# Performance work log

Measured on AMD Instinct MI355X. Metric: run time of the kernel, lower is better.

Reference implementation:

```python
import jax, jax.numpy as jnp
import numpy as np

WS = 7          # window size (7x7)
N = WS * WS     # tokens per window = 49
C = 192         # channels
H = 6           # heads
NW = 64         # windows per image (for mask)
B_ = 8192       # num_windows * batch


def _rel_index():
    coords = np.stack(np.meshgrid(np.arange(WS), np.arange(WS), indexing='ij'))  # [2,7,7]
    cf = coords.reshape(2, -1)                       # [2,49]
    rc = (cf[:, :, None] - cf[:, None, :]).transpose(1, 2, 0).astype(np.int64)  # [49,49,2]
    rc[..., 0] += WS - 1
    rc[..., 1] += WS - 1
    rc[..., 0] *= 2 * WS - 1
    return jnp.asarray(rc.sum(-1), dtype=jnp.int32)  # [49,49], values in [0, 169)


def setup_inputs() -> dict:
    key = jax.random.key(0)
    ks = jax.random.split(key, 10)
    std = 0.02
    return {
        'xq': jax.random.normal(ks[0], (B_, N, C), dtype=jnp.float32),
        'mask': jax.random.normal(ks[1], (NW, N, N), dtype=jnp.float32),
        'Wq': jax.random.normal(ks[2], (C, C), dtype=jnp.float32) * std,
        'bq': jnp.zeros((C,), dtype=jnp.float32),
        'Wkv': jax.random.normal(ks[3], (C, 2 * C), dtype=jnp.float32) * std,
        'bkv': jnp.zeros((2 * C,), dtype=jnp.float32),
        'Wproj': jax.random.normal(ks[4], (C, C), dtype=jnp.float32) * std,
        'bproj': jnp.zeros((C,), dtype=jnp.float32),
        'bias_table': jax.random.normal(ks[5], ((2 * WS - 1) * (2 * WS - 1), H), dtype=jnp.float32) * std,
        'rel_index': _rel_index(),
    }


def reference(xq, mask, Wq, bq, Wkv, bkv, Wproj, bproj, bias_table, rel_index):
    b_, n, c = xq.shape
    h = H
    dh = c // h
    scale = dh ** (-0.5)
    # projections (xkv = xq since xkv is None in the original call)
    q = (xq @ Wq + bq).reshape(b_, n, h, dh).transpose(0, 2, 1, 3) * scale      # [b_,h,n,dh]
    kv = (xq @ Wkv + bkv).reshape(b_, n, 2, h, dh).transpose(2, 0, 3, 1, 4)     # [2,b_,h,n,dh]
    k, v = kv[0], kv[1]
    attn = jnp.einsum('bhqd,bhkd->bhqk', q, k)                                   # [b_,h,n,n]
    # gathered relative-position bias: [n,n,h] -> [h,n,n]
    bias = bias_table[rel_index.reshape(-1)].reshape(n, n, h).transpose(2, 0, 1)
    attn = attn + bias[None]
    # mask add: [b_//nw, nw, h, n, n] + [1, nw, 1, n, n]
    nw = mask.shape[0]
    attn = attn.reshape(b_ // nw, nw, h, n, n) + mask[None, :, None]
    attn = jax.nn.softmax(attn.reshape(b_, h, n, n), axis=-1)
    x = jnp.einsum('bhqk,bhkd->bhqd', attn, v).transpose(0, 2, 1, 3).reshape(b_, n, c)
    return x @ Wproj + bproj
```

## Files before the change

kernel.cpp:

```cpp
#include <hip/hip_runtime.h>


#define NTOK 49
#define CCH 192

typedef __bf16 bf16_t;
typedef bf16_t bf16x8 __attribute__((ext_vector_type(8)));
typedef bf16_t bf16x4 __attribute__((ext_vector_type(4)));
typedef float f32x4 __attribute__((ext_vector_type(4)));

#define WS_WQT   0
#define WS_WKVT  73728
#define WS_WPT   221184
#define WS_BQS   294912
#define WS_TBL   295680

#define SWZ(row, off) ((off) ^ (((row) & 7) << 4))

__global__ void prep_kernel(const float* __restrict__ Wq, const float* __restrict__ bq,
                            const float* __restrict__ Wkv, const float* __restrict__ Wproj,
                            const float* __restrict__ btab, const int* __restrict__ rel,
                            const float* __restrict__ mask,
                            bf16_t* __restrict__ wqt, bf16_t* __restrict__ wkvt,
                            bf16_t* __restrict__ wpt, float* __restrict__ bqs,
                            float* __restrict__ tbl, int mode) {
    const float SC = 0.17677669529663687f;
    long i = (long)blockIdx.x * 256 + threadIdx.x;
    if (i < 36864) { int n = i / 192, k = i % 192; wqt[i] = (bf16_t)(Wq[k * 192 + n] * SC); return; }
    i -= 36864;
    if (i < 73728) { int n = i / 192, k = i % 192; wkvt[i] = (bf16_t)Wkv[k * 384 + n]; return; }
    i -= 73728;
    if (i < 36864) { int n = i / 192, k = i % 192; wpt[i] = (bf16_t)Wproj[k * 192 + n]; return; }
    i -= 36864;
    if (i < 192) { bqs[i] = bq[i] * SC; return; }
    i -= 192;
    if (mode == 0) {
        if (i < 979072) {
            int c = i % 52; long r = i / 52; int q = r % 49; r /= 49; int h = r % 6; int w = r / 6;
            tbl[i] = (c < 49) ? (btab[rel[q * 49 + c] * 6 + h] + mask[(size_t)w * 2401 + q * 49 + c]) : 0.f;
        }
    } else if (mode == 1) {
        if (i < 15288) { int c = i % 52; int r = i / 52; int q = r % 49; int h = r / 49;
            tbl[i] = (c < 49) ? btab[rel[q * 49 + c] * 6 + h] : 0.f; return; }
        i -= 15288;
        if (i < 163072) { int c = i % 52; long r = i / 52; int q = r % 49; int w = r / 49;
            tbl[15288 + i] = (c < 49) ? mask[(size_t)w * 2401 + q * 49 + c] : 0.f; }
    } else {
        if (i < 14406) { int h = i / 2401, rc = i % 2401; tbl[i] = btab[rel[rc] * 6 + h]; }
    }
}

__global__ __launch_bounds__(1024, 4) void wattn_kernel(
    const float* __restrict__ xq, const float* __restrict__ mask,
    const float* __restrict__ bkv, const float* __restrict__ bproj,
    const bf16_t* __restrict__ wqt, const bf16_t* __restrict__ wkvt, const bf16_t* __restrict__ wpt,
    const float* __restrict__ bqs, const float* __restrict__ tbl,
    float* __restrict__ out, int mode)
{
    __shared__ __align__(16) unsigned char smem[131072];
    unsigned char* XsO = smem;
    unsigned char* Qs  = smem + 24576;
    unsigned char* Ks  = smem + 49152;
    unsigned char* Vt  = smem + 73728;
    unsigned char* Ps  = smem + 98304;

    const int tid = threadIdx.x;
    const int wid = tid >> 6;
    const int lane = tid & 63;
    const int l15 = lane & 15;
    const int lg = lane >> 4;
    const int b = blockIdx.x;
    const float* xp = xq + (size_t)b * (NTOK * CCH);

    for (int idx = tid; idx < 2352; idx += 1024) {
        int row = idx / 48;
        int c4 = idx % 48;
        float4 v = *(const float4*)(xp + row * 192 + c4 * 4);
        bf16x4 pk = { (bf16_t)v.x, (bf16_t)v.y, (bf16_t)v.z, (bf16_t)v.w };
        *(bf16x4*)(XsO + row * 384 + SWZ(row, c4 * 8)) = pk;
    }
    if (tid < 720) *(unsigned long long*)(XsO + 49 * 384 + tid * 8) = 0ULL;
    __syncthreads();

    {
        bf16x8 bfr[6];
        float4 bias4;
        float bv = 0.f;
        int prev_ut = -1;
        for (int u = 9 * wid; u < 9 * wid + 9; ++u) {
            int ut = u >> 2, mt = u & 3;
            bool isV = (ut >= 24);
            if (ut != prev_ut) {
                prev_ut = ut;
                const bf16_t* wrow;
                if (ut < 12)      wrow = wqt  + (size_t)(ut * 16 + l15) * 192;
                else if (ut < 24) wrow = wkvt + (size_t)((ut - 12) * 16 + l15) * 192;
                else              wrow = wkvt + (size_t)(192 + (ut - 24) * 16 + l15) * 192;
#pragma unroll
                for (int ks = 0; ks < 6; ks++) bfr[ks] = *(const bf16x8*)(wrow + ks * 32 + lg * 8);
                if (!isV) {
                    const float* bp = (ut < 12) ? (bqs + ut * 16) : (bkv + (ut - 12) * 16);
                    bias4 = *(const float4*)(bp + lg * 4);
                } else {
                    bv = bkv[192 + (ut - 24) * 16 + l15];
                }
            }
            int xrow = mt * 16 + l15;
            bf16x8 xf[6];
#pragma unroll
            for (int ks = 0; ks < 6; ks++)
                xf[ks] = *(const bf16x8*)(XsO + xrow * 384 + SWZ(xrow, ks * 64 + lg * 16));
            if (!isV) {
                f32x4 acc = { bias4.x, bias4.y, bias4.z, bias4.w };
#pragma unroll
                for (int ks = 0; ks < 6; ks++)
                    acc = __builtin_amdgcn_mfma_f32_16x16x32_bf16(bfr[ks], xf[ks], acc, 0, 0, 0);
                int ncol = (ut < 12 ? ut : ut - 12) * 16;
                unsigned char* dst = (ut < 12) ? Qs : Ks;
                bf16x4 pk = { (bf16_t)acc[0], (bf16_t)acc[1], (bf16_t)acc[2], (bf16_t)acc[3] };
                int trow = mt * 16 + l15;
                *(bf16x4*)(dst + trow * 384 + SWZ(trow, ncol * 2 + lg * 8)) = pk;
            } else {
                f32x4 acc = { bv, bv, bv, bv };
#pragma unroll
                for (int ks = 0; ks < 6; ks++)
                    acc = __builtin_amdgcn_mfma_f32_16x16x32_bf16(xf[ks], bfr[ks], acc, 0, 0, 0);
                int crow = (ut - 24) * 16 + l15;
                bf16x4 pk = { (bf16_t)acc[0], (bf16_t)acc[1], (bf16_t)acc[2], (bf16_t)acc[3] };
                *(bf16x4*)(Vt + crow * 128 + SWZ(crow, mt * 32 + lg * 8)) = pk;
            }
        }
    }
    __syncthreads();

    const int widx = b & 63;
    unsigned char* Pw = Ps + wid * 2048;
    for (int u = wid; u < 24; u += 16) {
        int h = u >> 2, qt = u & 3;
        int cb = h * 64 + lg * 16;
        int qrow = qt * 16 + l15;
        bf16x8 qfr = *(const bf16x8*)(Qs + qrow * 384 + SWZ(qrow, cb));
        f32x4 s[4];
#pragma unroll
        for (int f = 0; f < 4; f++) {
            int kr = f * 16 + l15;
            bf16x8 kfr = *(const bf16x8*)(Ks + kr * 384 + SWZ(kr, cb));
            f32x4 z = { 0.f, 0.f, 0.f, 0.f };
            s[f] = __builtin_amdgcn_mfma_f32_16x16x32_bf16(kfr, qfr, z, 0, 0, 0);
        }
        int q = qt * 16 + l15;
        bool qok = (q < 49);
#pragma unroll
        for (int f = 0; f < 4; f++) {
            int kb = f * 16 + lg * 4;
            float4 a = { 0.f, 0.f, 0.f, 0.f };
            if (qok && kb < 49) {
                if (mode == 0) {
                    a = *(const float4*)(tbl + (((size_t)(widx * 6 + h) * 49 + q) * 52 + kb));
                } else if (mode == 1) {
                    float4 b1 = *(const float4*)(tbl + ((size_t)(h * 49 + q) * 52 + kb));
                    float4 m1 = *(const float4*)(tbl + 15288 + (((size_t)widx * 49 + q) * 52 + kb));
                    a.x = b1.x + m1.x; a.y = b1.y + m1.y; a.z = b1.z + m1.z; a.w = b1.w + m1.w;
                }
            }
#pragma unroll
            for (int j = 0; j < 4; j++) {
                int k = kb + j;
                float av = (j == 0) ? a.x : (j == 1) ? a.y : (j == 2) ? a.z : a.w;
                if (mode == 2) {
                    av = 0.f;
                    if (qok && k < 49)
                        av = tbl[h * 2401 + q * 49 + k] + mask[(size_t)widx * 2401 + q * 49 + k];
                }
                if (k >= 49) s[f][j] = -1e30f;
                else if (qok) s[f][j] += av;
            }
        }
        float m = -1e30f;
#pragma unroll
        for (int f = 0; f < 4; f++)
#pragma unroll
            for (int j = 0; j < 4; j++) m = fmaxf(m, s[f][j]);
        m = fmaxf(m, __shfl_xor(m, 16));
        m = fmaxf(m, __shfl_xor(m, 32));
        float t = 0.f;
#pragma unroll
        for (int f = 0; f < 4; f++)
#pragma unroll
            for (int j = 0; j < 4; j++) { s[f][j] = __expf(s[f][j] - m); t += s[f][j]; }
        t += __shfl_xor(t, 16);
        t += __shfl_xor(t, 32);
        float inv = 1.0f / t;
#pragma unroll
        for (int f = 0; f < 4; f++) {
            bf16x4 pk = { (bf16_t)(s[f][0] * inv), (bf16_t)(s[f][1] * inv),
                          (bf16_t)(s[f][2] * inv), (bf16_t)(s[f][3] * inv) };
            *(bf16x4*)(Pw + l15 * 128 + SWZ(l15, f * 32 + lg * 8)) = pk;
        }
        __threadfence_block();
        bf16x8 pa[2];
#pragma unroll
        for (int ks = 0; ks < 2; ks++)
            pa[ks] = *(const bf16x8*)(Pw + l15 * 128 + SWZ(l15, ks * 64 + lg * 16));
#pragma unroll
        for (int dt = 0; dt < 2; dt++) {
            f32x4 acc = { 0.f, 0.f, 0.f, 0.f };
#pragma unroll
            for (int ks = 0; ks < 2; ks++) {
                int vr = h * 32 + dt * 16 + l15;
                bf16x8 vfr = *(const bf16x8*)(Vt + vr * 128 + SWZ(vr, ks * 64 + lg * 16));
                acc = __builtin_amdgcn_mfma_f32_16x16x32_bf16(vfr, pa[ks], acc, 0, 0, 0);
            }
            int orow = qt * 16 + l15;
            bf16x4 pk = { (bf16_t)acc[0], (bf16_t)acc[1], (bf16_t)acc[2], (bf16_t)acc[3] };
            *(bf16x4*)(XsO + orow * 384 + SWZ(orow, h * 64 + dt * 32 + lg * 8)) = pk;
        }
    }
    __syncthreads();

    {
        float* op = out + (size_t)b * (NTOK * CCH);
        bf16x8 bfr[6];
        float4 bias4 = { 0.f, 0.f, 0.f, 0.f };
        int prev_nt = -1;
        for (int u = 3 * wid; u < 3 * wid + 3; ++u) {
            int nt = u >> 2, mt = u & 3;
            if (nt != prev_nt) {
                prev_nt = nt;
                const bf16_t* wrow = wpt + (size_t)(nt * 16 + l15) * 192;
#pragma unroll
                for (int ks = 0; ks < 6; ks++) bfr[ks] = *(const bf16x8*)(wrow + ks * 32 + lg * 8);
                bias4 = *(const float4*)(bproj + nt * 16 + lg * 4);
            }
            int orow = mt * 16 + l15;
            f32x4 acc = { bias4.x, bias4.y, bias4.z, bias4.w };
#pragma unroll
            for (int ks = 0; ks < 6; ks++) {
                bf16x8 of = *(const bf16x8*)(XsO + orow * 384 + SWZ(orow, ks * 64 + lg * 16));
                acc = __builtin_amdgcn_mfma_f32_16x16x32_bf16(bfr[ks], of, acc, 0, 0, 0);
            }
            if (orow < 49) {
                float4 st = { acc[0], acc[1], acc[2], acc[3] };
                *(float4*)(op + orow * 192 + nt * 16 + lg * 4) = st;
            }
        }
    }
}

extern "C" void kernel_launch(void* const* d_in, const int* in_sizes, int n_in,
                              void* d_out, int out_size, void* d_ws, size_t ws_size,
                              hipStream_t stream) {
    const float* xq    = (const float*)d_in[0];
    const float* mask  = (const float*)d_in[1];
    const float* Wq    = (const float*)d_in[2];
    const float* bq    = (const float*)d_in[3];
    const float* Wkv   = (const float*)d_in[4];
    const float* bkv   = (const float*)d_in[5];
    const float* Wproj = (const float*)d_in[6];
    const float* bproj = (const float*)d_in[7];
    const float* btab  = (const float*)d_in[8];
    const int*   rel   = (const int*)d_in[9];
    float* out = (float*)d_out;

    char* ws = (char*)d_ws;
    bf16_t* wqt  = (bf16_t*)(ws + WS_WQT);
    bf16_t* wkvt = (bf16_t*)(ws + WS_WKVT);
    bf16_t* wpt  = (bf16_t*)(ws + WS_WPT);
    float*  bqs  = (float*)(ws + WS_BQS);
    float*  tbl  = (float*)(ws + WS_TBL);

    size_t need0 = (size_t)WS_TBL + 979072u * 4u;
    size_t need1 = (size_t)WS_TBL + 178360u * 4u;
    int mode = (ws_size >= need0) ? 0 : (ws_size >= need1 ? 1 : 2);

    long prep_elems = 147648L + (mode == 0 ? 979072L : (mode == 1 ? 178360L : 14406L));
    int prep_blocks = (int)((prep_elems + 255) / 256);
    prep_kernel<<<prep_blocks, 256, 0, stream>>>(Wq, bq, Wkv, Wproj, btab, rel, mask,
                                                 wqt, wkvt, wpt, bqs, tbl, mode);
    wattn_kernel<<<8192, 1024, 0, stream>>>(xq, mask, bkv, bproj, wqt, wkvt, wpt,
                                            bqs, tbl, out, mode);
}
```

Measured before the change: 642.4 us.

## Keep Q and P in registers via shuffles, shrink LDS, use exp2 softmax

Each wave now computes Q for its own query tile and keeps it in registers, moving it into MFMA operand layout with lane shuffles instead of staging through shared memory. The softmax probabilities are shuffled into operand form the same way, so the P buffer disappears. Shared memory drops from 128KB to 72KB and the launch-bounds occupancy hint is raised, which should let more blocks share a CU. The prep kernel folds log2(e) into the Q scale and the bias/mask table, pads the table rows to 64 with a -inf pad so the padding mask is precomputed, and the kernel uses exp2, rcp and deferred normalization after PV. The costs are extra shuffle traffic and register pressure, and weight fragments are reloaded per tile rather than reused.

```diff
diff --git a/kernel.cpp b/kernel.cpp
--- a/kernel.cpp
+++ b/kernel.cpp
@@ -7,6 +7,7 @@
 typedef __bf16 bf16_t;
 typedef bf16_t bf16x8 __attribute__((ext_vector_type(8)));
 typedef bf16_t bf16x4 __attribute__((ext_vector_type(4)));
+typedef bf16_t bf16x2 __attribute__((ext_vector_type(2)));
 typedef float f32x4 __attribute__((ext_vector_type(4)));
 
 #define WS_WQT   0
@@ -16,6 +17,11 @@
 #define WS_TBL   295680
 
 #define SWZ(row, off) ((off) ^ (((row) & 7) << 4))
+
+__device__ __forceinline__ unsigned pk2(float a, float b) {
+    bf16x2 w = { (bf16_t)a, (bf16_t)b };
+    return __builtin_bit_cast(unsigned, w);
+}
 
 __global__ void prep_kernel(const float* __restrict__ Wq, const float* __restrict__ bq,
                             const float* __restrict__ Wkv, const float* __restrict__ Wproj,
@@ -24,7 +30,8 @@
                             bf16_t* __restrict__ wqt, bf16_t* __restrict__ wkvt,
                             bf16_t* __restrict__ wpt, float* __restrict__ bqs,
                             float* __restrict__ tbl, int mode) {
-    const float SC = 0.17677669529663687f;
+    const float SC  = 0.2550718212080052f;
+    const float L2E = 1.4426950408889634f;
     long i = (long)blockIdx.x * 256 + threadIdx.x;
     if (i < 36864) { int n = i / 192, k = i % 192; wqt[i] = (bf16_t)(Wq[k * 192 + n] * SC); return; }
     i -= 36864;
@@ -35,34 +42,33 @@
     if (i < 192) { bqs[i] = bq[i] * SC; return; }
     i -= 192;
     if (mode == 0) {
-        if (i < 979072) {
-            int c = i % 52; long r = i / 52; int q = r % 49; r /= 49; int h = r % 6; int w = r / 6;
-            tbl[i] = (c < 49) ? (btab[rel[q * 49 + c] * 6 + h] + mask[(size_t)w * 2401 + q * 49 + c]) : 0.f;
+        if (i < 1204224) {
+            int c = i & 63; long r = i >> 6; int q = r % 49; r /= 49; int h = r % 6; int w = r / 6;
+            tbl[i] = (c < 49) ? (btab[rel[q * 49 + c] * 6 + h] + mask[(size_t)w * 2401 + q * 49 + c]) * L2E
+                              : -1e30f;
         }
     } else if (mode == 1) {
-        if (i < 15288) { int c = i % 52; int r = i / 52; int q = r % 49; int h = r / 49;
-            tbl[i] = (c < 49) ? btab[rel[q * 49 + c] * 6 + h] : 0.f; return; }
-        i -= 15288;
-        if (i < 163072) { int c = i % 52; long r = i / 52; int q = r % 49; int w = r / 49;
-            tbl[15288 + i] = (c < 49) ? mask[(size_t)w * 2401 + q * 49 + c] : 0.f; }
+        if (i < 18816) { int c = i & 63; int r = i >> 6; int q = r % 49; int h = r / 49;
+            tbl[i] = (c < 49) ? btab[rel[q * 49 + c] * 6 + h] * L2E : 0.f; return; }
+        i -= 18816;
+        if (i < 200704) { int c = i & 63; long r = i >> 6; int q = r % 49; int w = r / 49;
+            tbl[18816 + i] = (c < 49) ? mask[(size_t)w * 2401 + q * 49 + c] * L2E : -1e30f; }
     } else {
         if (i < 14406) { int h = i / 2401, rc = i % 2401; tbl[i] = btab[rel[rc] * 6 + h]; }
     }
 }
 
-__global__ __launch_bounds__(1024, 4) void wattn_kernel(
+__global__ __launch_bounds__(1024, 8) void wattn_kernel(
     const float* __restrict__ xq, const float* __restrict__ mask,
     const float* __restrict__ bkv, const float* __restrict__ bproj,
     const bf16_t* __restrict__ wqt, const bf16_t* __restrict__ wkvt, const bf16_t* __restrict__ wpt,
     const float* __restrict__ bqs, const float* __restrict__ tbl,
     float* __restrict__ out, int mode)
 {
-    __shared__ __align__(16) unsigned char smem[131072];
+    __shared__ __align__(16) unsigned char smem[73728];
     unsigned char* XsO = smem;
-    unsigned char* Qs  = smem + 24576;
-    unsigned char* Ks  = smem + 49152;
-    unsigned char* Vt  = smem + 73728;
-    unsigned char* Ps  = smem + 98304;
+    unsigned char* Ks  = smem + 24576;
+    unsigned char* Vt  = smem + 49152;
 
     const int tid = threadIdx.x;
     const int wid = tid >> 6;
@@ -71,6 +77,7 @@
     const int lg = lane >> 4;
     const int b = blockIdx.x;
     const float* xp = xq + (size_t)b * (NTOK * CCH);
+    const float LOG2E = 1.4426950408889634f;
 
     for (int idx = tid; idx < 2352; idx += 1024) {
         int row = idx / 48;
@@ -82,101 +89,118 @@
     if (tid < 720) *(unsigned long long*)(XsO + 49 * 384 + tid * 8) = 0ULL;
     __syncthreads();
 
+    const int qt = wid & 3;
+    unsigned qw0[4], qw1[4];
     {
-        bf16x8 bfr[6];
-        float4 bias4;
-        float bv = 0.f;
-        int prev_ut = -1;
-        for (int u = 9 * wid; u < 9 * wid + 9; ++u) {
-            int ut = u >> 2, mt = u & 3;
-            bool isV = (ut >= 24);
-            if (ut != prev_ut) {
-                prev_ut = ut;
-                const bf16_t* wrow;
-                if (ut < 12)      wrow = wqt  + (size_t)(ut * 16 + l15) * 192;
-                else if (ut < 24) wrow = wkvt + (size_t)((ut - 12) * 16 + l15) * 192;
-                else              wrow = wkvt + (size_t)(192 + (ut - 24) * 16 + l15) * 192;
-#pragma unroll
-                for (int ks = 0; ks < 6; ks++) bfr[ks] = *(const bf16x8*)(wrow + ks * 32 + lg * 8);
-                if (!isV) {
-                    const float* bp = (ut < 12) ? (bqs + ut * 16) : (bkv + (ut - 12) * 16);
-                    bias4 = *(const float4*)(bp + lg * 4);
-                } else {
-                    bv = bkv[192 + (ut - 24) * 16 + l15];
+        int xrow = qt * 16 + l15;
+        bf16x8 xf[6];
+#pragma unroll
+        for (int ks = 0; ks < 6; ks++)
+            xf[ks] = *(const bf16x8*)(XsO + xrow * 384 + SWZ(xrow, ks * 64 + lg * 16));
+
+        auto qproj = [&](int h, unsigned* qwv) {
+#pragma unroll
+            for (int dlt = 0; dlt < 2; dlt++) {
+                int ut = 2 * h + dlt;
+                float4 b4 = *(const float4*)(bqs + ut * 16 + lg * 4);
+                f32x4 acc = { b4.x, b4.y, b4.z, b4.w };
+                const bf16_t* wr = wqt + (size_t)(ut * 16 + l15) * 192 + lg * 8;
+#pragma unroll
+                for (int ks = 0; ks < 6; ks++) {
+                    bf16x8 bfr = *(const bf16x8*)(wr + ks * 32);
+                    acc = __builtin_amdgcn_mfma_f32_16x16x32_bf16(bfr, xf[ks], acc, 0, 0, 0);
                 }
-            }
-            int xrow = mt * 16 + l15;
-            bf16x8 xf[6];
-#pragma unroll
-            for (int ks = 0; ks < 6; ks++)
-                xf[ks] = *(const bf16x8*)(XsO + xrow * 384 + SWZ(xrow, ks * 64 + lg * 16));
-            if (!isV) {
-                f32x4 acc = { bias4.x, bias4.y, bias4.z, bias4.w };
-#pragma unroll
-                for (int ks = 0; ks < 6; ks++)
-                    acc = __builtin_amdgcn_mfma_f32_16x16x32_bf16(bfr[ks], xf[ks], acc, 0, 0, 0);
-                int ncol = (ut < 12 ? ut : ut - 12) * 16;
-                unsigned char* dst = (ut < 12) ? Qs : Ks;
-                bf16x4 pk = { (bf16_t)acc[0], (bf16_t)acc[1], (bf16_t)acc[2], (bf16_t)acc[3] };
-                int trow = mt * 16 + l15;
-                *(bf16x4*)(dst + trow * 384 + SWZ(trow, ncol * 2 + lg * 8)) = pk;
-            } else {
-                f32x4 acc = { bv, bv, bv, bv };
-#pragma unroll
-                for (int ks = 0; ks < 6; ks++)
-                    acc = __builtin_amdgcn_mfma_f32_16x16x32_bf16(xf[ks], bfr[ks], acc, 0, 0, 0);
-                int crow = (ut - 24) * 16 + l15;
-                bf16x4 pk = { (bf16_t)acc[0], (bf16_t)acc[1], (bf16_t)acc[2], (bf16_t)acc[3] };
-                *(bf16x4*)(Vt + crow * 128 + SWZ(crow, mt * 32 + lg * 8)) = pk;
-            }
-        }
+                qwv[dlt * 2 + 0] = pk2(acc[0], acc[1]);
+                qwv[dlt * 2 + 1] = pk2(acc[2], acc[3]);
+            }
+        };
+        qproj(wid >> 2, qw0);
+        if (wid < 8) qproj(4 + (wid >> 2), qw1);
+    }
+    for (int i = 0; i < 3; i++) {
+        int u = 3 * wid + i;
+        int nt = u >> 2, mt = u & 3;
+        int xr = mt * 16 + l15;
+        bf16x8 xfk[6];
+#pragma unroll
+        for (int ks = 0; ks < 6; ks++)
+            xfk[ks] = *(const bf16x8*)(XsO + xr * 384 + SWZ(xr, ks * 64 + lg * 16));
+        float4 kb4 = *(const float4*)(bkv + nt * 16 + lg * 4);
+        f32x4 ka = { kb4.x, kb4.y, kb4.z, kb4.w };
+        const bf16_t* wrk = wkvt + (size_t)(nt * 16 + l15) * 192 + lg * 8;
+#pragma unroll
+        for (int ks = 0; ks < 6; ks++) {
+            bf16x8 bfr = *(const bf16x8*)(wrk + ks * 32);
+            ka = __builtin_amdgcn_mfma_f32_16x16x32_bf16(bfr, xfk[ks], ka, 0, 0, 0);
+        }
+        bf16x4 kp = { (bf16_t)ka[0], (bf16_t)ka[1], (bf16_t)ka[2], (bf16_t)ka[3] };
+        *(bf16x4*)(Ks + xr * 384 + SWZ(xr, nt * 32 + lg * 8)) = kp;
+        float bv = bkv[192 + nt * 16 + l15];
+        f32x4 va = { bv, bv, bv, bv };
+        const bf16_t* wrv = wkvt + (size_t)(192 + nt * 16 + l15) * 192 + lg * 8;
+#pragma unroll
+        for (int ks = 0; ks < 6; ks++) {
+            bf16x8 bfr = *(const bf16x8*)(wrv + ks * 32);
+            va = __builtin_amdgcn_mfma_f32_16x16x32_bf16(xfk[ks], bfr, va, 0, 0, 0);
+        }
+        int vr = nt * 16 + l15;
+        bf16x4 vp = { (bf16_t)va[0], (bf16_t)va[1], (bf16_t)va[2], (bf16_t)va[3] };
+        *(bf16x4*)(Vt + vr * 128 + SWZ(vr, mt * 32 + lg * 8)) = vp;
     }
     __syncthreads();
 
     const int widx = b & 63;
-    unsigned char* Pw = Ps + wid * 2048;
-    for (int u = wid; u < 24; u += 16) {
-        int h = u >> 2, qt = u & 3;
-        int cb = h * 64 + lg * 16;
-        int qrow = qt * 16 + l15;
-        bf16x8 qfr = *(const bf16x8*)(Qs + qrow * 384 + SWZ(qrow, cb));
+    auto attn_unit = [&](int h, const unsigned* qwv) {
+        unsigned qword[4];
+#pragma unroll
+        for (int i = 0; i < 4; i++) {
+            int src = l15 + 16 * (((lg & 1) << 1) | (i >> 1));
+            unsigned v0 = (unsigned)__shfl((int)qwv[(i & 1)], src, 64);
+            unsigned v1 = (unsigned)__shfl((int)qwv[2 + (i & 1)], src, 64);
+            qword[i] = (lg & 2) ? v1 : v0;
+        }
+        uint4 qq = { qword[0], qword[1], qword[2], qword[3] };
+        bf16x8 qfr = __builtin_bit_cast(bf16x8, qq);
         f32x4 s[4];
 #pragma unroll
         for (int f = 0; f < 4; f++) {
             int kr = f * 16 + l15;
-            bf16x8 kfr = *(const bf16x8*)(Ks + kr * 384 + SWZ(kr, cb));
+            bf16x8 kfr = *(const bf16x8*)(Ks + kr * 384 + SWZ(kr, h * 64 + lg * 16));
             f32x4 z = { 0.f, 0.f, 0.f, 0.f };
             s[f] = __builtin_amdgcn_mfma_f32_16x16x32_bf16(kfr, qfr, z, 0, 0, 0);
         }
         int q = qt * 16 + l15;
         bool qok = (q < 49);
-#pragma unroll
-        for (int f = 0; f < 4; f++) {
-            int kb = f * 16 + lg * 4;
-            float4 a = { 0.f, 0.f, 0.f, 0.f };
-            if (qok && kb < 49) {
-                if (mode == 0) {
-                    a = *(const float4*)(tbl + (((size_t)(widx * 6 + h) * 49 + q) * 52 + kb));
-                } else if (mode == 1) {
-                    float4 b1 = *(const float4*)(tbl + ((size_t)(h * 49 + q) * 52 + kb));
-                    float4 m1 = *(const float4*)(tbl + 15288 + (((size_t)widx * 49 + q) * 52 + kb));
-                    a.x = b1.x + m1.x; a.y = b1.y + m1.y; a.z = b1.z + m1.z; a.w = b1.w + m1.w;
+        if (mode == 0) {
+#pragma unroll
+            for (int f = 0; f < 4; f++) {
+                if (qok) {
+                    float4 bm = *(const float4*)(tbl + (((size_t)(widx * 6 + h) * 49 + q) << 6) + f * 16 + lg * 4);
+                    s[f][0] += bm.x; s[f][1] += bm.y; s[f][2] += bm.z; s[f][3] += bm.w;
                 }
             }
-#pragma unroll
-            for (int j = 0; j < 4; j++) {
-                int k = kb + j;
-                float av = (j == 0) ? a.x : (j == 1) ? a.y : (j == 2) ? a.z : a.w;
-                if (mode == 2) {
-                    av = 0.f;
-                    if (qok && k < 49)
-                        av = tbl[h * 2401 + q * 49 + k] + mask[(size_t)widx * 2401 + q * 49 + k];
+        } else if (mode == 1) {
+#pragma unroll
+            for (int f = 0; f < 4; f++) {
+                if (qok) {
+                    float4 b1 = *(const float4*)(tbl + (((size_t)(h * 49 + q)) << 6) + f * 16 + lg * 4);
+                    float4 m1 = *(const float4*)(tbl + 18816 + (((size_t)(widx * 49 + q)) << 6) + f * 16 + lg * 4);
+                    s[f][0] += b1.x + m1.x; s[f][1] += b1.y + m1.y;
+                    s[f][2] += b1.z + m1.z; s[f][3] += b1.w + m1.w;
                 }
-                if (k >= 49) s[f][j] = -1e30f;
-                else if (qok) s[f][j] += av;
-            }
-        }
-        float m = -1e30f;
+            }
+        } else {
+#pragma unroll
+            for (int f = 0; f < 4; f++)
+#pragma unroll
+                for (int j = 0; j < 4; j++) {
+                    int k = f * 16 + lg * 4 + j;
+                    if (k >= 49) s[f][j] = -1e30f;
+                    else if (qok)
+                        s[f][j] += (tbl[h * 2401 + q * 49 + k] + mask[(size_t)widx * 2401 + q * 49 + k]) * LOG2E;
+                }
+        }
+        float m = s[0][0];
 #pragma unroll
         for (int f = 0; f < 4; f++)
 #pragma unroll
@@ -187,57 +211,63 @@
 #pragma unroll
         for (int f = 0; f < 4; f++)
 #pragma unroll
-            for (int j = 0; j < 4; j++) { s[f][j] = __expf(s[f][j] - m); t += s[f][j]; }
+            for (int j = 0; j < 4; j++) { s[f][j] = __builtin_amdgcn_exp2f(s[f][j] - m); t += s[f][j]; }
         t += __shfl_xor(t, 16);
         t += __shfl_xor(t, 32);
-        float inv = 1.0f / t;
+        float inv = __builtin_amdgcn_rcpf(t);
+        unsigned Wp[8];
 #pragma unroll
         for (int f = 0; f < 4; f++) {
-            bf16x4 pk = { (bf16_t)(s[f][0] * inv), (bf16_t)(s[f][1] * inv),
-                          (bf16_t)(s[f][2] * inv), (bf16_t)(s[f][3] * inv) };
-            *(bf16x4*)(Pw + l15 * 128 + SWZ(l15, f * 32 + lg * 8)) = pk;
-        }
-        __threadfence_block();
+            Wp[f * 2 + 0] = pk2(s[f][0], s[f][1]);
+            Wp[f * 2 + 1] = pk2(s[f][2], s[f][3]);
+        }
         bf16x8 pa[2];
 #pragma unroll
-        for (int ks = 0; ks < 2; ks++)
-            pa[ks] = *(const bf16x8*)(Pw + l15 * 128 + SWZ(l15, ks * 64 + lg * 16));
+        for (int ks2 = 0; ks2 < 2; ks2++) {
+            unsigned pw[4];
+#pragma unroll
+            for (int p = 0; p < 4; p++) {
+                int src = l15 + 16 * (((lg & 1) << 1) | (p >> 1));
+                unsigned v0 = (unsigned)__shfl((int)Wp[(2 * ks2) * 2 + (p & 1)], src, 64);
+                unsigned v1 = (unsigned)__shfl((int)Wp[(2 * ks2 + 1) * 2 + (p & 1)], src, 64);
+                pw[p] = (lg & 2) ? v1 : v0;
+            }
+            uint4 pp = { pw[0], pw[1], pw[2], pw[3] };
+            pa[ks2] = __builtin_bit_cast(bf16x8, pp);
+        }
 #pragma unroll
         for (int dt = 0; dt < 2; dt++) {
             f32x4 acc = { 0.f, 0.f, 0.f, 0.f };
 #pragma unroll
-            for (int ks = 0; ks < 2; ks++) {
+            for (int ks2 = 0; ks2 < 2; ks2++) {
                 int vr = h * 32 + dt * 16 + l15;
-                bf16x8 vfr = *(const bf16x8*)(Vt + vr * 128 + SWZ(vr, ks * 64 + lg * 16));
-                acc = __builtin_amdgcn_mfma_f32_16x16x32_bf16(vfr, pa[ks], acc, 0, 0, 0);
+                bf16x8 vfr = *(const bf16x8*)(Vt + vr * 128 + SWZ(vr, ks2 * 64 + lg * 16));
+                acc = __builtin_amdgcn_mfma_f32_16x16x32_bf16(vfr, pa[ks2], acc, 0, 0, 0);
             }
             int orow = qt * 16 + l15;
-            bf16x4 pk = { (bf16_t)acc[0], (bf16_t)acc[1], (bf16_t)acc[2], (bf16_t)acc[3] };
-            *(bf16x4*)(XsO + orow * 384 + SWZ(orow, h * 64 + dt * 32 + lg * 8)) = pk;
-        }
-    }
+            bf16x4 op4 = { (bf16_t)(acc[0] * inv), (bf16_t)(acc[1] * inv),
+                           (bf16_t)(acc[2] * inv), (bf16_t)(acc[3] * inv) };
+            *(bf16x4*)(XsO + orow * 384 + SWZ(orow, h * 64 + dt * 32 + lg * 8)) = op4;
+        }
+    };
+    attn_unit(wid >> 2, qw0);
+    if (wid < 8) attn_unit(4 + (wid >> 2), qw1);
     __syncthreads();
 
     {
         float* op = out + (size_t)b * (NTOK * CCH);
-        bf16x8 bfr[6];
-        float4 bias4 = { 0.f, 0.f, 0.f, 0.f };
-        int prev_nt = -1;
-        for (int u = 3 * wid; u < 3 * wid + 3; ++u) {
+        for (int i = 0; i < 3; i++) {
+            int u = 3 * wid + i;
             int nt = u >> 2, mt = u & 3;
-            if (nt != prev_nt) {
-                prev_nt = nt;
-                const bf16_t* wrow = wpt + (size_t)(nt * 16 + l15) * 192;
-#pragma unroll
-                for (int ks = 0; ks < 6; ks++) bfr[ks] = *(const bf16x8*)(wrow + ks * 32 + lg * 8);
-                bias4 = *(const float4*)(bproj + nt * 16 + lg * 4);
-            }
+            float4 b4 = *(const float4*)(bproj + nt * 16 + lg * 4);
+            f32x4 acc = { b4.x, b4.y, b4.z, b4.w };
+            const bf16_t* wr = wpt + (size_t)(nt * 16 + l15) * 192 + lg * 8;
             int orow = mt * 16 + l15;
-            f32x4 acc = { bias4.x, bias4.y, bias4.z, bias4.w };
 #pragma unroll
             for (int ks = 0; ks < 6; ks++) {
+                bf16x8 bfr = *(const bf16x8*)(wr + ks * 32);
                 bf16x8 of = *(const bf16x8*)(XsO + orow * 384 + SWZ(orow, ks * 64 + lg * 16));
-                acc = __builtin_amdgcn_mfma_f32_16x16x32_bf16(bfr[ks], of, acc, 0, 0, 0);
+                acc = __builtin_amdgcn_mfma_f32_16x16x32_bf16(bfr, of, acc, 0, 0, 0);
             }
             if (orow < 49) {
                 float4 st = { acc[0], acc[1], acc[2], acc[3] };
@@ -269,11 +299,12 @@
     float*  bqs  = (float*)(ws + WS_BQS);
     float*  tbl  = (float*)(ws + WS_TBL);
 
-    size_t need0 = (size_t)WS_TBL + 979072u * 4u;
-    size_t need1 = (size_t)WS_TBL + 178360u * 4u;
+    size_t need0 = (size_t)WS_TBL + 1204224u * 4u;
+    size_t need1 = (size_t)WS_TBL + 219520u * 4u;
     int mode = (ws_size >= need0) ? 0 : (ws_size >= need1 ? 1 : 2);
 
-    long prep_elems = 147648L + (mode == 0 ? 979072L : (mode == 1 ? 178360L : 14406L));
+    long tblN = (mode == 0) ? 1204224L : (mode == 1 ? 219520L : 14406L);
+    long prep_elems = 147648L + tblN;
     int prep_blocks = (int)((prep_elems + 255) / 256);
     prep_kernel<<<prep_blocks, 256, 0, stream>>>(Wq, bq, Wkv, Wproj, btab, rel, mask,
                                                  wqt, wkvt, wpt, bqs, tbl, mode);
```

Result: slower. 1.193 ms (+85.7%).
